# Kernel tuning notes

Hardware: AMD Instinct MI355X
Metric: run time of the kernel (lower is better)

Reference implementation:

```python
import jax, jax.numpy as jnp
import numpy as np

ALPHA_U = 1.0 / 10.0   # dt/tauu
ALPHA_V = 1.0 / 150.0  # dt/tauv
M = 10.0

def setup_inputs() -> dict:
    key = jax.random.key(0)
    ks = jax.random.split(key, 6)
    B, D_in, H = 8192, 1024, 2048
    stdv = 1.0 / np.sqrt(H)
    return {
        "x": jax.random.normal(ks[0], (B, D_in), dtype=jnp.float32),
        "u": jax.random.normal(ks[1], (B, H), dtype=jnp.float32),
        "v": jax.random.normal(ks[2], (B, H), dtype=jnp.float32),
        "win": jax.random.uniform(ks[3], (H, D_in), dtype=jnp.float32, minval=-stdv, maxval=stdv),
        "wr": jax.random.uniform(ks[4], (H, H), dtype=jnp.float32, minval=-stdv, maxval=stdv),
        "bias": jax.random.uniform(ks[5], (H,), dtype=jnp.float32, minval=-stdv, maxval=stdv),
    }

def reference(x, u, v, win, wr, bias):
    # v update: leaky blend toward m*u, then relu
    v_new = jax.nn.relu((1.0 - ALPHA_V) * v + (ALPHA_V * M) * u)
    # u update: leaky blend with input + recurrent drive minus adapted v
    drive = jnp.einsum('bi,hi->bh', x, win) + jnp.einsum('bk,hk->bh', u, wr) + bias - v_new
    u_new = jax.nn.relu((1.0 - ALPHA_U) * u + ALPHA_U * drive)
    return (u_new, v_new)
```

## Files before the change

### kernel.cpp

```cpp
#include <hip/hip_runtime.h>
#include <hip/hip_bf16.h>
#include <stdint.h>

#define B_DIM 8192
#define D_IN  1024
#define H_DIM 2048
#define K_DIM (D_IN + H_DIM)

#define CV_CONST  (1.0f - 1.0f/150.0f)
#define CUV_CONST (10.0f/150.0f)
#define CU_CONST  0.9f
#define AU_CONST  0.1f

typedef __attribute__((ext_vector_type(8))) short short8;
typedef __attribute__((ext_vector_type(4))) float floatx4;

__device__ __forceinline__ unsigned short f2bf(float f) {
    union { float f; unsigned u; } x; x.f = f;
    unsigned r = x.u + 0x7fffu + ((x.u >> 16) & 1u);
    return (unsigned short)(r >> 16);
}

#define N4_X   ((B_DIM * D_IN)  / 4)
#define N4_U   ((B_DIM * H_DIM) / 4)
#define N4_WIN ((H_DIM * D_IN)  / 4)
#define N4_WR  ((H_DIM * H_DIM) / 4)
#define N4_TOT (N4_X + N4_U + N4_WIN + N4_WR)

__global__ __launch_bounds__(256)
void pack_all(const float4* __restrict__ x, const float4* __restrict__ u,
              const float4* __restrict__ win, const float4* __restrict__ wr,
              unsigned short* __restrict__ Abf, unsigned short* __restrict__ Wbf) {
    int i = blockIdx.x * 256 + threadIdx.x;
    const float4* src; unsigned short* dst; int shift, mask, coloff;
    if (i < N4_X)                    { src = x;   dst = Abf; shift = 10; mask = 1023; coloff = 0;    }
    else if (i < N4_X + N4_U)        { i -= N4_X; src = u;   dst = Abf; shift = 11; mask = 2047; coloff = D_IN; }
    else if (i < N4_X + N4_U + N4_WIN){ i -= N4_X + N4_U; src = win; dst = Wbf; shift = 10; mask = 1023; coloff = 0; }
    else                             { i -= N4_X + N4_U + N4_WIN; src = wr; dst = Wbf; shift = 11; mask = 2047; coloff = D_IN; }
    int idx = i << 2;
    int r = idx >> shift;
    int c = idx & mask;
    float4 f = src[i];
    ushort4 o;
    o.x = f2bf(f.x); o.y = f2bf(f.y); o.z = f2bf(f.z); o.w = f2bf(f.w);
    *(ushort4*)(dst + (size_t)r * K_DIM + coloff + c) = o;
}

#define GLOAD_LDS16(gp, lp)                                                          \
    __builtin_amdgcn_global_load_lds(                                                \
        (const __attribute__((address_space(1))) unsigned int*)(gp),                 \
        (__attribute__((address_space(3))) unsigned int*)(lp), 16, 0, 0)

#define VMCNT(n)  asm volatile("s_waitcnt vmcnt(" #n ")" ::: "memory")
#define LGKM0     asm volatile("s_waitcnt lgkmcnt(0)" ::: "memory")
#define SCHEDB    __builtin_amdgcn_sched_barrier(0)
#define BAR       __builtin_amdgcn_s_barrier()
#define PRIO1     __builtin_amdgcn_s_setprio(1)
#define PRIO0     __builtin_amdgcn_s_setprio(0)

#define NT (K_DIM / 64)

#define ALO 0
#define BLO 16384
#define BHI 32768
#define AHI 49152

#define ES_STRIDE 68
#define ES_REGION (16 * ES_STRIDE)

__global__ __launch_bounds__(512, 2)
void gemm_fused(const unsigned short* __restrict__ A,
                const unsigned short* __restrict__ Wc,
                const float* __restrict__ u_in,
                const float* __restrict__ v_in,
                const float* __restrict__ bias,
                float* __restrict__ out)
{
    __shared__ __align__(16) unsigned char smem[131072];

    const int tid  = threadIdx.x;
    const int wave = tid >> 6;
    const int lane = tid & 63;
    const int wrh  = wave >> 2;
    const int wc   = wave & 3;

    const int bid   = blockIdx.x;
    const int wid   = ((bid & 7) << 5) | (bid >> 3);
    const int tileM = (wid >> 3) << 8;
    const int tileN = (wid & 7)  << 8;

    const int frow = lane & 15;
    const int g    = lane >> 4;

    const unsigned short* Ag = A  + (size_t)(tileM + (wave >> 1) * 16 + frow) * K_DIM
                                  + (wave & 1) * 32 + g * 8;
    const unsigned short* Bg = Wc + (size_t)(tileN + (wave >> 2) * 64 + ((wave >> 1) & 1) * 16 + frow) * K_DIM
                                  + (wave & 1) * 32 + g * 8;
    const size_t R128 = (size_t)128 * K_DIM;
    const size_t R64  = (size_t) 64 * K_DIM;
    const size_t R32  = (size_t) 32 * K_DIM;

    const int w1024 = wave << 10;

    const int aRd = (wrh << 13) + (lane << 4);
    const int bRd = (wc  << 12) + (lane << 4);

    GLOAD_LDS16(Ag,               smem + ALO + w1024);
    GLOAD_LDS16(Ag + R128,        smem + ALO + 8192 + w1024);
    GLOAD_LDS16(Bg,               smem + BLO + w1024);
    GLOAD_LDS16(Bg + R128,        smem + BLO + 8192 + w1024);
    GLOAD_LDS16(Bg + R32,         smem + BHI + w1024);
    GLOAD_LDS16(Bg + R32 + R128,  smem + BHI + 8192 + w1024);
    GLOAD_LDS16(Ag + R64,         smem + AHI + w1024);
    GLOAD_LDS16(Ag + R64 + R128,  smem + AHI + 8192 + w1024);

    VMCNT(4);
    BAR;
    LGKM0;

    floatx4 acc[8][4] = {};
    short8 Ar[4][2], Bl[2][2], Bh[2][2];

#define RD_A(cb, unit, i2s) (*(const short8*)(smem + (cb) + (unit) + aRd + (i2s) * 1024))
#define RD_B(cb, unit, j2s) (*(const short8*)(smem + (cb) + (unit) + bRd + (j2s) * 1024))

#pragma clang loop unroll(disable)
    for (int t = 0; t < NT - 1; ++t) {
        const int cb = (t & 1) << 16;
        const int nb = cb ^ 65536;
        const size_t kk = (size_t)(t + 1) * 64;

        GLOAD_LDS16(Ag + kk,        smem + nb + ALO + w1024);
        GLOAD_LDS16(Ag + kk + R128, smem + nb + ALO + 8192 + w1024);
#pragma unroll
        for (int i = 0; i < 4; ++i) { Ar[i][0] = RD_A(cb, ALO, i*2); Ar[i][1] = RD_A(cb, ALO, i*2+1); }
#pragma unroll
        for (int j = 0; j < 2; ++j) { Bl[j][0] = RD_B(cb, BLO, j*2); Bl[j][1] = RD_B(cb, BLO, j*2+1); }
        VMCNT(4);
        BAR; LGKM0; SCHEDB;
        PRIO1;
#pragma unroll
        for (int i = 0; i < 4; ++i)
#pragma unroll
            for (int j = 0; j < 2; ++j) {
                acc[i][j] = __builtin_amdgcn_mfma_f32_16x16x32_bf16(Ar[i][0], Bl[j][0], acc[i][j], 0, 0, 0);
                acc[i][j] = __builtin_amdgcn_mfma_f32_16x16x32_bf16(Ar[i][1], Bl[j][1], acc[i][j], 0, 0, 0);
            }
        PRIO0; SCHEDB;
        BAR;

        GLOAD_LDS16(Bg + kk,        smem + nb + BLO + w1024);
        GLOAD_LDS16(Bg + kk + R128, smem + nb + BLO + 8192 + w1024);
#pragma unroll
        for (int j = 0; j < 2; ++j) { Bh[j][0] = RD_B(cb, BHI, j*2); Bh[j][1] = RD_B(cb, BHI, j*2+1); }
        VMCNT(4);
        BAR; LGKM0; SCHEDB;
        PRIO1;
#pragma unroll
        for (int i = 0; i < 4; ++i)
#pragma unroll
            for (int j = 0; j < 2; ++j) {
                acc[i][2+j] = __builtin_amdgcn_mfma_f32_16x16x32_bf16(Ar[i][0], Bh[j][0], acc[i][2+j], 0, 0, 0);
                acc[i][2+j] = __builtin_amdgcn_mfma_f32_16x16x32_bf16(Ar[i][1], Bh[j][1], acc[i][2+j], 0, 0, 0);
            }
        PRIO0; SCHEDB;
        BAR;

        GLOAD_LDS16(Bg + kk + R32,        smem + nb + BHI + w1024);
        GLOAD_LDS16(Bg + kk + R32 + R128, smem + nb + BHI + 8192 + w1024);
#pragma unroll
        for (int i = 0; i < 4; ++i) { Ar[i][0] = RD_A(cb, AHI, i*2); Ar[i][1] = RD_A(cb, AHI, i*2+1); }
        BAR; LGKM0; SCHEDB;
        PRIO1;
#pragma unroll
        for (int i = 0; i < 4; ++i)
#pragma unroll
            for (int j = 0; j < 2; ++j) {
                acc[4+i][2+j] = __builtin_amdgcn_mfma_f32_16x16x32_bf16(Ar[i][0], Bh[j][0], acc[4+i][2+j], 0, 0, 0);
                acc[4+i][2+j] = __builtin_amdgcn_mfma_f32_16x16x32_bf16(Ar[i][1], Bh[j][1], acc[4+i][2+j], 0, 0, 0);
            }
        PRIO0; SCHEDB;
        BAR;

        GLOAD_LDS16(Ag + kk + R64,        smem + nb + AHI + w1024);
        GLOAD_LDS16(Ag + kk + R64 + R128, smem + nb + AHI + 8192 + w1024);
        VMCNT(4);
        BAR; LGKM0; SCHEDB;
        PRIO1;
#pragma unroll
        for (int i = 0; i < 4; ++i)
#pragma unroll
            for (int j = 0; j < 2; ++j) {
                acc[4+i][j] = __builtin_amdgcn_mfma_f32_16x16x32_bf16(Ar[i][0], Bl[j][0], acc[4+i][j], 0, 0, 0);
                acc[4+i][j] = __builtin_amdgcn_mfma_f32_16x16x32_bf16(Ar[i][1], Bl[j][1], acc[4+i][j], 0, 0, 0);
            }
        PRIO0; SCHEDB;
        BAR;
    }

    {
        const int cb = ((NT - 1) & 1) << 16;
#pragma unroll
        for (int i = 0; i < 4; ++i) { Ar[i][0] = RD_A(cb, ALO, i*2); Ar[i][1] = RD_A(cb, ALO, i*2+1); }
#pragma unroll
        for (int j = 0; j < 2; ++j) { Bl[j][0] = RD_B(cb, BLO, j*2); Bl[j][1] = RD_B(cb, BLO, j*2+1); }
        VMCNT(2);
        BAR; LGKM0; SCHEDB;
        PRIO1;
#pragma unroll
        for (int i = 0; i < 4; ++i)
#pragma unroll
            for (int j = 0; j < 2; ++j) {
                acc[i][j] = __builtin_amdgcn_mfma_f32_16x16x32_bf16(Ar[i][0], Bl[j][0], acc[i][j], 0, 0, 0);
                acc[i][j] = __builtin_amdgcn_mfma_f32_16x16x32_bf16(Ar[i][1], Bl[j][1], acc[i][j], 0, 0, 0);
            }
        PRIO0; SCHEDB;
        BAR;
#pragma unroll
        for (int j = 0; j < 2; ++j) { Bh[j][0] = RD_B(cb, BHI, j*2); Bh[j][1] = RD_B(cb, BHI, j*2+1); }
        VMCNT(0);
        BAR; LGKM0; SCHEDB;
        PRIO1;
#pragma unroll
        for (int i = 0; i < 4; ++i)
#pragma unroll
            for (int j = 0; j < 2; ++j) {
                acc[i][2+j] = __builtin_amdgcn_mfma_f32_16x16x32_bf16(Ar[i][0], Bh[j][0], acc[i][2+j], 0, 0, 0);
                acc[i][2+j] = __builtin_amdgcn_mfma_f32_16x16x32_bf16(Ar[i][1], Bh[j][1], acc[i][2+j], 0, 0, 0);
            }
        PRIO0; SCHEDB;
        BAR;
#pragma unroll
        for (int i = 0; i < 4; ++i) { Ar[i][0] = RD_A(cb, AHI, i*2); Ar[i][1] = RD_A(cb, AHI, i*2+1); }
        BAR; LGKM0; SCHEDB;
        PRIO1;
#pragma unroll
        for (int i = 0; i < 4; ++i)
#pragma unroll
            for (int j = 0; j < 2; ++j) {
                acc[4+i][2+j] = __builtin_amdgcn_mfma_f32_16x16x32_bf16(Ar[i][0], Bh[j][0], acc[4+i][2+j], 0, 0, 0);
                acc[4+i][2+j] = __builtin_amdgcn_mfma_f32_16x16x32_bf16(Ar[i][1], Bh[j][1], acc[4+i][2+j], 0, 0, 0);
            }
        PRIO0; SCHEDB;
        BAR;
        PRIO1;
#pragma unroll
        for (int i = 0; i < 4; ++i)
#pragma unroll
            for (int j = 0; j < 2; ++j) {
                acc[4+i][j] = __builtin_amdgcn_mfma_f32_16x16x32_bf16(Ar[i][0], Bl[j][0], acc[4+i][j], 0, 0, 0);
                acc[4+i][j] = __builtin_amdgcn_mfma_f32_16x16x32_bf16(Ar[i][1], Bl[j][1], acc[4+i][j], 0, 0, 0);
            }
        PRIO0;
    }

    __syncthreads();

    float* Esf = (float*)smem;
    const int q    = lane >> 4;
    const int c16  = lane & 15;
    const int colg = tileN + wc * 64 + c16 * 4;
    const float4 b4 = *(const float4*)&bias[colg];
    const size_t outV = (size_t)B_DIM * H_DIM;

#pragma unroll
    for (int i = 0; i < 8; ++i) {
        float* Es = Esf + (wave * 2 + (i & 1)) * ES_REGION;
#pragma unroll
        for (int j = 0; j < 4; ++j)
#pragma unroll
            for (int r = 0; r < 4; ++r)
                Es[(q * 4 + r) * ES_STRIDE + j * 16 + c16] = acc[i][j][r];
#pragma unroll
        for (int rg = 0; rg < 4; rg++) {
            const int rloc = rg * 4 + q;
            const float4 a4 = *(const float4*)&Es[rloc * ES_STRIDE + c16 * 4];
            const size_t idx = (size_t)(tileM + wrh * 128 + i * 16 + rloc) * H_DIM + colg;
            const float4 u4 = *(const float4*)&u_in[idx];
            const float4 v4 = *(const float4*)&v_in[idx];
            float4 vn, un;
            vn.x = fmaxf(CV_CONST * v4.x + CUV_CONST * u4.x, 0.0f);
            vn.y = fmaxf(CV_CONST * v4.y + CUV_CONST * u4.y, 0.0f);
            vn.z = fmaxf(CV_CONST * v4.z + CUV_CONST * u4.z, 0.0f);
            vn.w = fmaxf(CV_CONST * v4.w + CUV_CONST * u4.w, 0.0f);
            un.x = fmaxf(CU_CONST * u4.x + AU_CONST * (a4.x + b4.x - vn.x), 0.0f);
            un.y = fmaxf(CU_CONST * u4.y + AU_CONST * (a4.y + b4.y - vn.y), 0.0f);
            un.z = fmaxf(CU_CONST * u4.z + AU_CONST * (a4.z + b4.z - vn.z), 0.0f);
            un.w = fmaxf(CU_CONST * u4.w + AU_CONST * (a4.w + b4.w - vn.w), 0.0f);
            *(float4*)&out[idx]        = un;
            *(float4*)&out[outV + idx] = vn;
        }
    }
}

extern "C" void kernel_launch(void* const* d_in, const int* in_sizes, int n_in,
                              void* d_out, int out_size, void* d_ws, size_t ws_size,
                              hipStream_t stream) {
    const float* x    = (const float*)d_in[0];
    const float* u    = (const float*)d_in[1];
    const float* v    = (const float*)d_in[2];
    const float* win  = (const float*)d_in[3];
    const float* wr   = (const float*)d_in[4];
    const float* bias = (const float*)d_in[5];
    float* out = (float*)d_out;

    unsigned short* Abf = (unsigned short*)d_ws;
    unsigned short* Wbf = Abf + (size_t)B_DIM * K_DIM;

    pack_all<<<N4_TOT / 256, 256, 0, stream>>>(
        (const float4*)x, (const float4*)u, (const float4*)win, (const float4*)wr,
        Abf, Wbf);

    gemm_fused<<<256, 512, 0, stream>>>(Abf, Wbf, u, v, bias, out);
}
```

Measured before the change: 373.9 us.

## Collapse four-phase ping-pong K loop into one barrier per K step

Replaces the four sub-phase schedule, where each 64-wide K step was split into quadrants with interleaved global loads, LDS reads and barriers, with a single phase. All eight next-tile global-to-LDS loads are issued up front, then one wait and barrier, then every A and B fragment is read into registers, and all 64 MFMAs run back to back. The loop is also unrolled by two. This cuts per-iteration barrier and wait overhead but holds more fragment registers (separate Alo/Ahi) and loses the fine-grained overlap of LDS reads with MFMA.

```diff
diff --git a/kernel.cpp b/kernel.cpp
--- a/kernel.cpp
+++ b/kernel.cpp
@@ -114,142 +114,102 @@
     GLOAD_LDS16(Ag + R64,         smem + AHI + w1024);
     GLOAD_LDS16(Ag + R64 + R128,  smem + AHI + 8192 + w1024);
 
-    VMCNT(4);
-    BAR;
-    LGKM0;
-
     floatx4 acc[8][4] = {};
-    short8 Ar[4][2], Bl[2][2], Bh[2][2];
+    short8 Alo[4][2], Ahi[4][2], Bl[2][2], Bh[2][2];
 
 #define RD_A(cb, unit, i2s) (*(const short8*)(smem + (cb) + (unit) + aRd + (i2s) * 1024))
 #define RD_B(cb, unit, j2s) (*(const short8*)(smem + (cb) + (unit) + bRd + (j2s) * 1024))
 
-#pragma clang loop unroll(disable)
+#pragma unroll 2
     for (int t = 0; t < NT - 1; ++t) {
         const int cb = (t & 1) << 16;
         const int nb = cb ^ 65536;
         const size_t kk = (size_t)(t + 1) * 64;
 
-        GLOAD_LDS16(Ag + kk,        smem + nb + ALO + w1024);
-        GLOAD_LDS16(Ag + kk + R128, smem + nb + ALO + 8192 + w1024);
-#pragma unroll
-        for (int i = 0; i < 4; ++i) { Ar[i][0] = RD_A(cb, ALO, i*2); Ar[i][1] = RD_A(cb, ALO, i*2+1); }
-#pragma unroll
-        for (int j = 0; j < 2; ++j) { Bl[j][0] = RD_B(cb, BLO, j*2); Bl[j][1] = RD_B(cb, BLO, j*2+1); }
-        VMCNT(4);
-        BAR; LGKM0; SCHEDB;
-        PRIO1;
-#pragma unroll
-        for (int i = 0; i < 4; ++i)
-#pragma unroll
-            for (int j = 0; j < 2; ++j) {
-                acc[i][j] = __builtin_amdgcn_mfma_f32_16x16x32_bf16(Ar[i][0], Bl[j][0], acc[i][j], 0, 0, 0);
-                acc[i][j] = __builtin_amdgcn_mfma_f32_16x16x32_bf16(Ar[i][1], Bl[j][1], acc[i][j], 0, 0, 0);
-            }
-        PRIO0; SCHEDB;
-        BAR;
-
-        GLOAD_LDS16(Bg + kk,        smem + nb + BLO + w1024);
-        GLOAD_LDS16(Bg + kk + R128, smem + nb + BLO + 8192 + w1024);
-#pragma unroll
-        for (int j = 0; j < 2; ++j) { Bh[j][0] = RD_B(cb, BHI, j*2); Bh[j][1] = RD_B(cb, BHI, j*2+1); }
-        VMCNT(4);
-        BAR; LGKM0; SCHEDB;
-        PRIO1;
-#pragma unroll
-        for (int i = 0; i < 4; ++i)
-#pragma unroll
-            for (int j = 0; j < 2; ++j) {
-                acc[i][2+j] = __builtin_amdgcn_mfma_f32_16x16x32_bf16(Ar[i][0], Bh[j][0], acc[i][2+j], 0, 0, 0);
-                acc[i][2+j] = __builtin_amdgcn_mfma_f32_16x16x32_bf16(Ar[i][1], Bh[j][1], acc[i][2+j], 0, 0, 0);
-            }
-        PRIO0; SCHEDB;
-        BAR;
-
+        GLOAD_LDS16(Ag + kk,              smem + nb + ALO + w1024);
+        GLOAD_LDS16(Ag + kk + R128,       smem + nb + ALO + 8192 + w1024);
+        GLOAD_LDS16(Bg + kk,              smem + nb + BLO + w1024);
+        GLOAD_LDS16(Bg + kk + R128,       smem + nb + BLO + 8192 + w1024);
         GLOAD_LDS16(Bg + kk + R32,        smem + nb + BHI + w1024);
         GLOAD_LDS16(Bg + kk + R32 + R128, smem + nb + BHI + 8192 + w1024);
-#pragma unroll
-        for (int i = 0; i < 4; ++i) { Ar[i][0] = RD_A(cb, AHI, i*2); Ar[i][1] = RD_A(cb, AHI, i*2+1); }
-        BAR; LGKM0; SCHEDB;
-        PRIO1;
-#pragma unroll
-        for (int i = 0; i < 4; ++i)
-#pragma unroll
-            for (int j = 0; j < 2; ++j) {
-                acc[4+i][2+j] = __builtin_amdgcn_mfma_f32_16x16x32_bf16(Ar[i][0], Bh[j][0], acc[4+i][2+j], 0, 0, 0);
-                acc[4+i][2+j] = __builtin_amdgcn_mfma_f32_16x16x32_bf16(Ar[i][1], Bh[j][1], acc[4+i][2+j], 0, 0, 0);
-            }
-        PRIO0; SCHEDB;
-        BAR;
-
         GLOAD_LDS16(Ag + kk + R64,        smem + nb + AHI + w1024);
         GLOAD_LDS16(Ag + kk + R64 + R128, smem + nb + AHI + 8192 + w1024);
-        VMCNT(4);
-        BAR; LGKM0; SCHEDB;
+
+        VMCNT(8);
+        BAR;
+        SCHEDB;
+
+#pragma unroll
+        for (int i = 0; i < 4; ++i) { Alo[i][0] = RD_A(cb, ALO, i*2); Alo[i][1] = RD_A(cb, ALO, i*2+1); }
+#pragma unroll
+        for (int j = 0; j < 2; ++j) { Bl[j][0] = RD_B(cb, BLO, j*2); Bl[j][1] = RD_B(cb, BLO, j*2+1); }
+#pragma unroll
+        for (int j = 0; j < 2; ++j) { Bh[j][0] = RD_B(cb, BHI, j*2); Bh[j][1] = RD_B(cb, BHI, j*2+1); }
+#pragma unroll
+        for (int i = 0; i < 4; ++i) { Ahi[i][0] = RD_A(cb, AHI, i*2); Ahi[i][1] = RD_A(cb, AHI, i*2+1); }
+
         PRIO1;
 #pragma unroll
         for (int i = 0; i < 4; ++i)
 #pragma unroll
             for (int j = 0; j < 2; ++j) {
-                acc[4+i][j] = __builtin_amdgcn_mfma_f32_16x16x32_bf16(Ar[i][0], Bl[j][0], acc[4+i][j], 0, 0, 0);
-                acc[4+i][j] = __builtin_amdgcn_mfma_f32_16x16x32_bf16(Ar[i][1], Bl[j][1], acc[4+i][j], 0, 0, 0);
-            }
-        PRIO0; SCHEDB;
+                acc[i][j] = __builtin_amdgcn_mfma_f32_16x16x32_bf16(Alo[i][0], Bl[j][0], acc[i][j], 0, 0, 0);
+                acc[i][j] = __builtin_amdgcn_mfma_f32_16x16x32_bf16(Alo[i][1], Bl[j][1], acc[i][j], 0, 0, 0);
+            }
+#pragma unroll
+        for (int i = 0; i < 4; ++i)
+#pragma unroll
+            for (int j = 0; j < 2; ++j) {
+                acc[i][2+j] = __builtin_amdgcn_mfma_f32_16x16x32_bf16(Alo[i][0], Bh[j][0], acc[i][2+j], 0, 0, 0);
+                acc[i][2+j] = __builtin_amdgcn_mfma_f32_16x16x32_bf16(Alo[i][1], Bh[j][1], acc[i][2+j], 0, 0, 0);
+            }
+#pragma unroll
+        for (int i = 0; i < 4; ++i)
+#pragma unroll
+            for (int j = 0; j < 2; ++j) {
+                acc[4+i][2+j] = __builtin_amdgcn_mfma_f32_16x16x32_bf16(Ahi[i][0], Bh[j][0], acc[4+i][2+j], 0, 0, 0);
+                acc[4+i][2+j] = __builtin_amdgcn_mfma_f32_16x16x32_bf16(Ahi[i][1], Bh[j][1], acc[4+i][2+j], 0, 0, 0);
+            }
+#pragma unroll
+        for (int i = 0; i < 4; ++i)
+#pragma unroll
+            for (int j = 0; j < 2; ++j) {
+                acc[4+i][j] = __builtin_amdgcn_mfma_f32_16x16x32_bf16(Ahi[i][0], Bl[j][0], acc[4+i][j], 0, 0, 0);
+                acc[4+i][j] = __builtin_amdgcn_mfma_f32_16x16x32_bf16(Ahi[i][1], Bl[j][1], acc[4+i][j], 0, 0, 0);
+            }
+        PRIO0;
+
+        LGKM0;
         BAR;
     }
 
     {
         const int cb = ((NT - 1) & 1) << 16;
-#pragma unroll
-        for (int i = 0; i < 4; ++i) { Ar[i][0] = RD_A(cb, ALO, i*2); Ar[i][1] = RD_A(cb, ALO, i*2+1); }
+        VMCNT(0);
+        BAR;
+        SCHEDB;
+#pragma unroll
+        for (int i = 0; i < 4; ++i) { Alo[i][0] = RD_A(cb, ALO, i*2); Alo[i][1] = RD_A(cb, ALO, i*2+1); }
 #pragma unroll
         for (int j = 0; j < 2; ++j) { Bl[j][0] = RD_B(cb, BLO, j*2); Bl[j][1] = RD_B(cb, BLO, j*2+1); }
-        VMCNT(2);
-        BAR; LGKM0; SCHEDB;
+#pragma unroll
+        for (int j = 0; j < 2; ++j) { Bh[j][0] = RD_B(cb, BHI, j*2); Bh[j][1] = RD_B(cb, BHI, j*2+1); }
+#pragma unroll
+        for (int i = 0; i < 4; ++i) { Ahi[i][0] = RD_A(cb, AHI, i*2); Ahi[i][1] = RD_A(cb, AHI, i*2+1); }
+
         PRIO1;
 #pragma unroll
         for (int i = 0; i < 4; ++i)
 #pragma unroll
             for (int j = 0; j < 2; ++j) {
-                acc[i][j] = __builtin_amdgcn_mfma_f32_16x16x32_bf16(Ar[i][0], Bl[j][0], acc[i][j], 0, 0, 0);
-                acc[i][j] = __builtin_amdgcn_mfma_f32_16x16x32_bf16(Ar[i][1], Bl[j][1], acc[i][j], 0, 0, 0);
-            }
-        PRIO0; SCHEDB;
-        BAR;
-#pragma unroll
-        for (int j = 0; j < 2; ++j) { Bh[j][0] = RD_B(cb, BHI, j*2); Bh[j][1] = RD_B(cb, BHI, j*2+1); }
-        VMCNT(0);
-        BAR; LGKM0; SCHEDB;
-        PRIO1;
-#pragma unroll
-        for (int i = 0; i < 4; ++i)
-#pragma unroll
-            for (int j = 0; j < 2; ++j) {
-                acc[i][2+j] = __builtin_amdgcn_mfma_f32_16x16x32_bf16(Ar[i][0], Bh[j][0], acc[i][2+j], 0, 0, 0);
-                acc[i][2+j] = __builtin_amdgcn_mfma_f32_16x16x32_bf16(Ar[i][1], Bh[j][1], acc[i][2+j], 0, 0, 0);
-            }
-        PRIO0; SCHEDB;
-        BAR;
-#pragma unroll
-        for (int i = 0; i < 4; ++i) { Ar[i][0] = RD_A(cb, AHI, i*2); Ar[i][1] = RD_A(cb, AHI, i*2+1); }
-        BAR; LGKM0; SCHEDB;
-        PRIO1;
-#pragma unroll
-        for (int i = 0; i < 4; ++i)
-#pragma unroll
-            for (int j = 0; j < 2; ++j) {
-                acc[4+i][2+j] = __builtin_amdgcn_mfma_f32_16x16x32_bf16(Ar[i][0], Bh[j][0], acc[4+i][2+j], 0, 0, 0);
-                acc[4+i][2+j] = __builtin_amdgcn_mfma_f32_16x16x32_bf16(Ar[i][1], Bh[j][1], acc[4+i][2+j], 0, 0, 0);
-            }
-        PRIO0; SCHEDB;
-        BAR;
-        PRIO1;
-#pragma unroll
-        for (int i = 0; i < 4; ++i)
-#pragma unroll
-            for (int j = 0; j < 2; ++j) {
-                acc[4+i][j] = __builtin_amdgcn_mfma_f32_16x16x32_bf16(Ar[i][0], Bl[j][0], acc[4+i][j], 0, 0, 0);
-                acc[4+i][j] = __builtin_amdgcn_mfma_f32_16x16x32_bf16(Ar[i][1], Bl[j][1], acc[4+i][j], 0, 0, 0);
+                acc[i][j]     = __builtin_amdgcn_mfma_f32_16x16x32_bf16(Alo[i][0], Bl[j][0], acc[i][j],     0, 0, 0);
+                acc[i][j]     = __builtin_amdgcn_mfma_f32_16x16x32_bf16(Alo[i][1], Bl[j][1], acc[i][j],     0, 0, 0);
+                acc[i][2+j]   = __builtin_amdgcn_mfma_f32_16x16x32_bf16(Alo[i][0], Bh[j][0], acc[i][2+j],   0, 0, 0);
+                acc[i][2+j]   = __builtin_amdgcn_mfma_f32_16x16x32_bf16(Alo[i][1], Bh[j][1], acc[i][2+j],   0, 0, 0);
+                acc[4+i][2+j] = __builtin_amdgcn_mfma_f32_16x16x32_bf16(Ahi[i][0], Bh[j][0], acc[4+i][2+j], 0, 0, 0);
+                acc[4+i][2+j] = __builtin_amdgcn_mfma_f32_16x16x32_bf16(Ahi[i][1], Bh[j][1], acc[4+i][2+j], 0, 0, 0);
+                acc[4+i][j]   = __builtin_amdgcn_mfma_f32_16x16x32_bf16(Ahi[i][0], Bl[j][0], acc[4+i][j],   0, 0, 0);
+                acc[4+i][j]   = __builtin_amdgcn_mfma_f32_16x16x32_bf16(Ahi[i][1], Bl[j][1], acc[4+i][j],   0, 0, 0);
             }
         PRIO0;
     }
```

Result: slower. 389.3 us (+4.1%).

## Batch per-tile LDS prefetches and cut barriers from eight to two per k-step

Applied to the files above, without the earlier changes.

The k-loop now issues the global-to-LDS loads for the A-low and both B halves together at the top of each step. It also reads the Bl, Ar and Bh fragments up front and uses partial lgkmcnt waits, so the first MFMA group can start while the later LDS reads are still in flight. The four barrier-separated MFMA phases are merged, leaving one barrier after the vmcnt wait and one at the end of the iteration. The epilogue is reworked the same way. This cuts synchronisation stalls in the 512-thread workgroup, at the cost of more outstanding memory operations and tighter ordering assumptions around the double-buffered LDS.

```diff
diff --git a/kernel.cpp b/kernel.cpp
--- a/kernel.cpp
+++ b/kernel.cpp
@@ -52,7 +52,7 @@
         (__attribute__((address_space(3))) unsigned int*)(lp), 16, 0, 0)
 
 #define VMCNT(n)  asm volatile("s_waitcnt vmcnt(" #n ")" ::: "memory")
-#define LGKM0     asm volatile("s_waitcnt lgkmcnt(0)" ::: "memory")
+#define LGKM(n)   asm volatile("s_waitcnt lgkmcnt(" #n ")" ::: "memory")
 #define SCHEDB    __builtin_amdgcn_sched_barrier(0)
 #define BAR       __builtin_amdgcn_s_barrier()
 #define PRIO1     __builtin_amdgcn_s_setprio(1)
@@ -113,10 +113,8 @@
     GLOAD_LDS16(Bg + R32 + R128,  smem + BHI + 8192 + w1024);
     GLOAD_LDS16(Ag + R64,         smem + AHI + w1024);
     GLOAD_LDS16(Ag + R64 + R128,  smem + AHI + 8192 + w1024);
-
-    VMCNT(4);
+    VMCNT(2);
     BAR;
-    LGKM0;
 
     floatx4 acc[8][4] = {};
     short8 Ar[4][2], Bl[2][2], Bh[2][2];
@@ -130,14 +128,25 @@
         const int nb = cb ^ 65536;
         const size_t kk = (size_t)(t + 1) * 64;
 
-        GLOAD_LDS16(Ag + kk,        smem + nb + ALO + w1024);
-        GLOAD_LDS16(Ag + kk + R128, smem + nb + ALO + 8192 + w1024);
+        GLOAD_LDS16(Ag + kk,              smem + nb + ALO + w1024);
+        GLOAD_LDS16(Ag + kk + R128,       smem + nb + ALO + 8192 + w1024);
+        GLOAD_LDS16(Bg + kk,              smem + nb + BLO + w1024);
+        GLOAD_LDS16(Bg + kk + R128,       smem + nb + BLO + 8192 + w1024);
+        GLOAD_LDS16(Bg + kk + R32,        smem + nb + BHI + w1024);
+        GLOAD_LDS16(Bg + kk + R32 + R128, smem + nb + BHI + 8192 + w1024);
+
+#pragma unroll
+        for (int j = 0; j < 2; ++j) { Bl[j][0] = RD_B(cb, BLO, j*2); Bl[j][1] = RD_B(cb, BLO, j*2+1); }
 #pragma unroll
         for (int i = 0; i < 4; ++i) { Ar[i][0] = RD_A(cb, ALO, i*2); Ar[i][1] = RD_A(cb, ALO, i*2+1); }
 #pragma unroll
-        for (int j = 0; j < 2; ++j) { Bl[j][0] = RD_B(cb, BLO, j*2); Bl[j][1] = RD_B(cb, BLO, j*2+1); }
-        VMCNT(4);
-        BAR; LGKM0; SCHEDB;
+        for (int j = 0; j < 2; ++j) { Bh[j][0] = RD_B(cb, BHI, j*2); Bh[j][1] = RD_B(cb, BHI, j*2+1); }
+
+        VMCNT(6);
+        BAR;
+        SCHEDB;
+
+        LGKM(4); SCHEDB;
         PRIO1;
 #pragma unroll
         for (int i = 0; i < 4; ++i)
@@ -146,15 +155,9 @@
                 acc[i][j] = __builtin_amdgcn_mfma_f32_16x16x32_bf16(Ar[i][0], Bl[j][0], acc[i][j], 0, 0, 0);
                 acc[i][j] = __builtin_amdgcn_mfma_f32_16x16x32_bf16(Ar[i][1], Bl[j][1], acc[i][j], 0, 0, 0);
             }
-        PRIO0; SCHEDB;
-        BAR;
-
-        GLOAD_LDS16(Bg + kk,        smem + nb + BLO + w1024);
-        GLOAD_LDS16(Bg + kk + R128, smem + nb + BLO + 8192 + w1024);
-#pragma unroll
-        for (int j = 0; j < 2; ++j) { Bh[j][0] = RD_B(cb, BHI, j*2); Bh[j][1] = RD_B(cb, BHI, j*2+1); }
-        VMCNT(4);
-        BAR; LGKM0; SCHEDB;
+        PRIO0;
+
+        LGKM(0); SCHEDB;
         PRIO1;
 #pragma unroll
         for (int i = 0; i < 4; ++i)
@@ -163,14 +166,14 @@
                 acc[i][2+j] = __builtin_amdgcn_mfma_f32_16x16x32_bf16(Ar[i][0], Bh[j][0], acc[i][2+j], 0, 0, 0);
                 acc[i][2+j] = __builtin_amdgcn_mfma_f32_16x16x32_bf16(Ar[i][1], Bh[j][1], acc[i][2+j], 0, 0, 0);
             }
-        PRIO0; SCHEDB;
-        BAR;
-
-        GLOAD_LDS16(Bg + kk + R32,        smem + nb + BHI + w1024);
-        GLOAD_LDS16(Bg + kk + R32 + R128, smem + nb + BHI + 8192 + w1024);
+        PRIO0;
+
+        GLOAD_LDS16(Ag + kk + R64,        smem + nb + AHI + w1024);
+        GLOAD_LDS16(Ag + kk + R64 + R128, smem + nb + AHI + 8192 + w1024);
 #pragma unroll
         for (int i = 0; i < 4; ++i) { Ar[i][0] = RD_A(cb, AHI, i*2); Ar[i][1] = RD_A(cb, AHI, i*2+1); }
-        BAR; LGKM0; SCHEDB;
+
+        LGKM(0); SCHEDB;
         PRIO1;
 #pragma unroll
         for (int i = 0; i < 4; ++i)
@@ -179,14 +182,6 @@
                 acc[4+i][2+j] = __builtin_amdgcn_mfma_f32_16x16x32_bf16(Ar[i][0], Bh[j][0], acc[4+i][2+j], 0, 0, 0);
                 acc[4+i][2+j] = __builtin_amdgcn_mfma_f32_16x16x32_bf16(Ar[i][1], Bh[j][1], acc[4+i][2+j], 0, 0, 0);
             }
-        PRIO0; SCHEDB;
-        BAR;
-
-        GLOAD_LDS16(Ag + kk + R64,        smem + nb + AHI + w1024);
-        GLOAD_LDS16(Ag + kk + R64 + R128, smem + nb + AHI + 8192 + w1024);
-        VMCNT(4);
-        BAR; LGKM0; SCHEDB;
-        PRIO1;
 #pragma unroll
         for (int i = 0; i < 4; ++i)
 #pragma unroll
@@ -194,18 +189,24 @@
                 acc[4+i][j] = __builtin_amdgcn_mfma_f32_16x16x32_bf16(Ar[i][0], Bl[j][0], acc[4+i][j], 0, 0, 0);
                 acc[4+i][j] = __builtin_amdgcn_mfma_f32_16x16x32_bf16(Ar[i][1], Bl[j][1], acc[4+i][j], 0, 0, 0);
             }
-        PRIO0; SCHEDB;
+        PRIO0;
+
+        VMCNT(2);
         BAR;
     }
 
     {
         const int cb = ((NT - 1) & 1) << 16;
 #pragma unroll
+        for (int j = 0; j < 2; ++j) { Bl[j][0] = RD_B(cb, BLO, j*2); Bl[j][1] = RD_B(cb, BLO, j*2+1); }
+#pragma unroll
         for (int i = 0; i < 4; ++i) { Ar[i][0] = RD_A(cb, ALO, i*2); Ar[i][1] = RD_A(cb, ALO, i*2+1); }
 #pragma unroll
-        for (int j = 0; j < 2; ++j) { Bl[j][0] = RD_B(cb, BLO, j*2); Bl[j][1] = RD_B(cb, BLO, j*2+1); }
-        VMCNT(2);
-        BAR; LGKM0; SCHEDB;
+        for (int j = 0; j < 2; ++j) { Bh[j][0] = RD_B(cb, BHI, j*2); Bh[j][1] = RD_B(cb, BHI, j*2+1); }
+        VMCNT(0);
+        BAR;
+        SCHEDB;
+        LGKM(4); SCHEDB;
         PRIO1;
 #pragma unroll
         for (int i = 0; i < 4; ++i)
@@ -214,12 +215,8 @@
                 acc[i][j] = __builtin_amdgcn_mfma_f32_16x16x32_bf16(Ar[i][0], Bl[j][0], acc[i][j], 0, 0, 0);
                 acc[i][j] = __builtin_amdgcn_mfma_f32_16x16x32_bf16(Ar[i][1], Bl[j][1], acc[i][j], 0, 0, 0);
             }
-        PRIO0; SCHEDB;
-        BAR;
-#pragma unroll
-        for (int j = 0; j < 2; ++j) { Bh[j][0] = RD_B(cb, BHI, j*2); Bh[j][1] = RD_B(cb, BHI, j*2+1); }
-        VMCNT(0);
-        BAR; LGKM0; SCHEDB;
+        PRIO0;
+        LGKM(0); SCHEDB;
         PRIO1;
 #pragma unroll
         for (int i = 0; i < 4; ++i)
@@ -228,11 +225,10 @@
                 acc[i][2+j] = __builtin_amdgcn_mfma_f32_16x16x32_bf16(Ar[i][0], Bh[j][0], acc[i][2+j], 0, 0, 0);
                 acc[i][2+j] = __builtin_amdgcn_mfma_f32_16x16x32_bf16(Ar[i][1], Bh[j][1], acc[i][2+j], 0, 0, 0);
             }
-        PRIO0; SCHEDB;
-        BAR;
+        PRIO0;
 #pragma unroll
         for (int i = 0; i < 4; ++i) { Ar[i][0] = RD_A(cb, AHI, i*2); Ar[i][1] = RD_A(cb, AHI, i*2+1); }
-        BAR; LGKM0; SCHEDB;
+        LGKM(0); SCHEDB;
         PRIO1;
 #pragma unroll
         for (int i = 0; i < 4; ++i)
@@ -240,16 +236,8 @@
             for (int j = 0; j < 2; ++j) {
                 acc[4+i][2+j] = __builtin_amdgcn_mfma_f32_16x16x32_bf16(Ar[i][0], Bh[j][0], acc[4+i][2+j], 0, 0, 0);
                 acc[4+i][2+j] = __builtin_amdgcn_mfma_f32_16x16x32_bf16(Ar[i][1], Bh[j][1], acc[4+i][2+j], 0, 0, 0);
-            }
-        PRIO0; SCHEDB;
-        BAR;
-        PRIO1;
-#pragma unroll
-        for (int i = 0; i < 4; ++i)
-#pragma unroll
-            for (int j = 0; j < 2; ++j) {
-                acc[4+i][j] = __builtin_amdgcn_mfma_f32_16x16x32_bf16(Ar[i][0], Bl[j][0], acc[4+i][j], 0, 0, 0);
-                acc[4+i][j] = __builtin_amdgcn_mfma_f32_16x16x32_bf16(Ar[i][1], Bl[j][1], acc[4+i][j], 0, 0, 0);
+                acc[4+i][j]   = __builtin_amdgcn_mfma_f32_16x16x32_bf16(Ar[i][0], Bl[j][0], acc[4+i][j],   0, 0, 0);
+                acc[4+i][j]   = __builtin_amdgcn_mfma_f32_16x16x32_bf16(Ar[i][1], Bl[j][1], acc[4+i][j],   0, 0, 0);
             }
         PRIO0;
     }
```

Measured after the change: 377.3 us. No clear change (+0.9%).
